# Kernel optimization log

Hardware: AMD Instinct MI355X
Metric: run time of the kernel (lower is better)

The kernel has to match this reference:

```python
import jax, jax.numpy as jnp
import numpy as np

B, D, H, W, K = 32, 256, 32, 32, 2048
BETA = 0.25
JSD_TS = 1.0


def setup_inputs() -> dict:
    key = jax.random.key(0)
    k1, k2 = jax.random.split(key)
    z = jax.random.normal(k1, (B, D, H, W), dtype=jnp.float32)
    # nn.Embedding(K, D) with uniform(-1/K, 1/K) init
    codebook = jax.random.uniform(k2, (K, D), minval=-1.0 / K, maxval=1.0 / K, dtype=jnp.float32)
    return {"z": z, "codebook": codebook, "i": 0, "it": 0}


def _vq_forward(z, codebook):
    b, d, h, w = z.shape
    # (b, d, h, w) -> (b*h*w, d)
    z_flat = jnp.transpose(z, (0, 2, 3, 1)).reshape(-1, d)
    # squared euclidean distances via sum-of-squares + matmul: (n, K)
    dist = (jnp.sum(z_flat * z_flat, axis=1, keepdims=True)
            + jnp.sum(codebook * codebook, axis=1)
            - 2.0 * (z_flat @ codebook.T))
    min_idx = jnp.argmin(dist, axis=1)                      # (n,)
    distance_prob = jax.nn.softmax(-dist / JSD_TS, axis=1)  # (n, K)
    z_q = codebook[min_idx]                                 # embedding gather (n, d)
    # VQ losses (normalize == 'none' so z_norm == z_flat)
    codebook_loss = jnp.mean((z_q - jax.lax.stop_gradient(z_flat)) ** 2)
    commitment_loss = jnp.mean((z_flat - jax.lax.stop_gradient(z_q)) ** 2)
    q_loss = codebook_loss + BETA * commitment_loss
    # straight-through estimator
    z_q = z_flat + jax.lax.stop_gradient(z_q - z_flat)
    z_q = jnp.transpose(z_q.reshape(b, h, w, d), (0, 3, 1, 2))
    return z_q, q_loss, distance_prob


def reference(z, codebook, i, it):
    # i, it are unused loop counters in the original forward (eval path)
    return _vq_forward(z, codebook)
```

## Files before the change

### kernel.cpp

```cpp
#include <hip/hip_runtime.h>
#include <stdint.h>

#define K_CODES 2048
#define DIM 256
#define NROWS 32768
#define ROWS_PER_BLOCK 16
#define THREADS 512
#define HW_STRIDE 1024
#define QLOSS_OFFSET 8388608
#define PROB_OFFSET 8388609ULL
#define ZB_PITCH 264
#define NBLOCKS (NROWS / ROWS_PER_BLOCK)
#define CPX (NBLOCKS / 8)

typedef short v8s __attribute__((ext_vector_type(8)));
typedef float v4f __attribute__((ext_vector_type(4)));
typedef __fp16 v2h __attribute__((ext_vector_type(2)));

__device__ __forceinline__ ushort f2bf(float x) {
    uint32_t u = __float_as_uint(x);
    return (ushort)((u + 0x7FFFu + ((u >> 16) & 1u)) >> 16);
}

__global__ void prep_kernel(const float* __restrict__ cb, ushort* __restrict__ cbb,
                            float* __restrict__ cnorm, float* __restrict__ qloss) {
    const int code = blockIdx.x;
    const int lane = threadIdx.x;
    float4 v = ((const float4*)(cb + code * DIM))[lane];
    ushort4 o;
    o.x = f2bf(v.x); o.y = f2bf(v.y); o.z = f2bf(v.z); o.w = f2bf(v.w);
    ((ushort4*)(cbb + code * DIM))[lane] = o;
    float ss = v.x * v.x + v.y * v.y + v.z * v.z + v.w * v.w;
    #pragma unroll
    for (int m = 32; m >= 1; m >>= 1) ss += __shfl_xor(ss, m, 64);
    if (lane == 0) cnorm[code] = ss;
    if (code == 0 && lane == 0) *qloss = 0.f;
}

__launch_bounds__(THREADS, 4)
__global__ void vq_kernel(const float* __restrict__ z, const float* __restrict__ cb,
                          const ushort* __restrict__ cbb, const float* __restrict__ cnorm,
                          float* __restrict__ out) {
    __shared__ float zf[DIM * 16];
    __shared__ ushort zb[ROWS_PER_BLOCK * ZB_PITCH];
    __shared__ float red_sum[8][16];
    __shared__ float red_val[8][16];
    __shared__ int   red_code[8][16];
    __shared__ float row_sum[16];
    __shared__ int   row_idx[16];
    __shared__ float lred[8];

    const int t = threadIdx.x;
    const int bid = ((int)blockIdx.x & 7) * CPX + ((int)blockIdx.x >> 3);
    const int n0 = bid * ROWS_PER_BLOCK;
    const int bb = n0 >> 10;
    const int hw = n0 & 1023;
    const float* zbase = z + (size_t)bb * (DIM * HW_STRIDE) + hw;

    #pragma unroll
    for (int j = 0; j < 2; ++j) {
        int i4 = t + j * THREADS;
        int d = i4 >> 2, m0 = (i4 & 3) << 2;
        float4 v = *(const float4*)(zbase + (size_t)d * HW_STRIDE + m0);
        *(float4*)&zf[d * 16 + m0] = v;
    }
    __syncthreads();
    #pragma unroll
    for (int j = 0; j < 4; ++j) {
        int i2 = t + j * THREADS;
        int m = i2 & 15, kp = i2 >> 4;
        float a0 = zf[(2 * kp) * 16 + m];
        float a1 = zf[(2 * kp + 1) * 16 + m];
        uint32_t pk = (uint32_t)f2bf(a0) | ((uint32_t)f2bf(a1) << 16);
        *(uint32_t*)&zb[m * ZB_PITCH + 2 * kp] = pk;
    }
    __syncthreads();

    const int wave = t >> 6, lane = t & 63;
    const int q = lane >> 4, lm = lane & 15;
    const int c0 = wave * 256;

    v8s afrag[8];
    const ushort* arow = &zb[lm * ZB_PITCH + q * 8];
    #pragma unroll
    for (int ks = 0; ks < 8; ++ks) afrag[ks] = *(const v8s*)(arow + ks * 32);

    float cnr[16];
    #pragma unroll
    for (int ct = 0; ct < 16; ++ct) cnr[ct] = cnorm[c0 + ct * 16 + lm];

    const ushort* bptr = cbb + (size_t)(c0 + lm) * DIM + q * 8;
    v8s bb0[8];
    #pragma unroll
    for (int ks = 0; ks < 8; ++ks) bb0[ks] = *(const v8s*)(bptr + ks * 32);

    v2h ep[32];
    float sume[4] = {0.f, 0.f, 0.f, 0.f};
    float bval[4] = {-1e30f, -1e30f, -1e30f, -1e30f};
    int   bcode[4] = {0, 0, 0, 0};
    #pragma unroll
    for (int ct = 0; ct < 16; ++ct) {
        v8s bb1[8];
        if (ct < 15) {
            const ushort* np = bptr + (size_t)(ct + 1) * (16 * DIM);
            #pragma unroll
            for (int ks = 0; ks < 8; ++ks) bb1[ks] = *(const v8s*)(np + ks * 32);
        }
        v4f a = {0.f, 0.f, 0.f, 0.f};
        #pragma unroll
        for (int ks = 0; ks < 8; ++ks)
            a = __builtin_amdgcn_mfma_f32_16x16x32_bf16(afrag[ks], bb0[ks], a, 0, 0, 0);
        const float cn = cnr[ct];
        const int code = c0 + ct * 16 + lm;
        #pragma unroll
        for (int r = 0; r < 4; ++r) {
            float l = 2.f * a[r] - cn;
            float ev = __expf(l);
            sume[r] += ev;
            if (l > bval[r]) { bval[r] = l; bcode[r] = code; }
            a[r] = ev;
        }
        ep[2 * ct]     = __builtin_amdgcn_cvt_pkrtz(a[0], a[1]);
        ep[2 * ct + 1] = __builtin_amdgcn_cvt_pkrtz(a[2], a[3]);
        #pragma unroll
        for (int ks = 0; ks < 8; ++ks) bb0[ks] = bb1[ks];
    }
    #pragma unroll
    for (int m = 1; m <= 8; m <<= 1) {
        #pragma unroll
        for (int r = 0; r < 4; ++r) {
            sume[r] += __shfl_xor(sume[r], m, 64);
            float v2 = __shfl_xor(bval[r], m, 64);
            int   c2 = __shfl_xor(bcode[r], m, 64);
            if (v2 > bval[r] || (v2 == bval[r] && c2 < bcode[r])) { bval[r] = v2; bcode[r] = c2; }
        }
    }
    if (lm == 0) {
        #pragma unroll
        for (int r = 0; r < 4; ++r) {
            red_sum[wave][q * 4 + r]  = sume[r];
            red_val[wave][q * 4 + r]  = bval[r];
            red_code[wave][q * 4 + r] = bcode[r];
        }
    }
    __syncthreads();
    if (t < 16) {
        float s = 0.f, bv = -1e30f;
        int bc = 0;
        #pragma unroll
        for (int w = 0; w < 8; ++w) {
            s += red_sum[w][t];
            float v = red_val[w][t];
            int   c = red_code[w][t];
            if (v > bv || (v == bv && c < bc)) { bv = v; bc = c; }
        }
        row_sum[t] = s;
        row_idx[t] = bc;
    }
    __syncthreads();

    float rinv[4];
    #pragma unroll
    for (int r = 0; r < 4; ++r) rinv[r] = 1.f / row_sum[q * 4 + r];
    float* prob = out + PROB_OFFSET;
    #pragma unroll
    for (int ct = 0; ct < 16; ++ct) {
        int col = c0 + ct * 16 + lm;
        float e0 = (float)ep[2 * ct][0];
        float e1 = (float)ep[2 * ct][1];
        float e2 = (float)ep[2 * ct + 1][0];
        float e3 = (float)ep[2 * ct + 1][1];
        size_t base = (size_t)(n0 + q * 4) * K_CODES + col;
        __builtin_nontemporal_store(e0 * rinv[0], prob + base);
        __builtin_nontemporal_store(e1 * rinv[1], prob + base + K_CODES);
        __builtin_nontemporal_store(e2 * rinv[2], prob + base + 2 * K_CODES);
        __builtin_nontemporal_store(e3 * rinv[3], prob + base + 3 * K_CODES);
    }

    float lacc = 0.f;
    #pragma unroll
    for (int j = 0; j < 2; ++j) {
        int i4 = t + j * THREADS;
        int d = i4 >> 2, m0 = (i4 & 3) << 2;
        float ov[4];
        #pragma unroll
        for (int i = 0; i < 4; ++i) {
            int m = m0 + i;
            float cv = cb[row_idx[m] * DIM + d];
            float zv = zf[d * 16 + m];
            float df = zv - cv;
            lacc += df * df;
            ov[i] = cv;
        }
        v4f o4 = {ov[0], ov[1], ov[2], ov[3]};
        __builtin_nontemporal_store(
            o4, (v4f*)(out + (size_t)bb * (DIM * HW_STRIDE) + hw + (size_t)d * HW_STRIDE + m0));
    }
    #pragma unroll
    for (int m = 32; m >= 1; m >>= 1) lacc += __shfl_xor(lacc, m, 64);
    if (lane == 0) lred[wave] = lacc;
    __syncthreads();
    if (t == 0) {
        float s = 0.f;
        #pragma unroll
        for (int w = 0; w < 8; ++w) s += lred[w];
        atomicAdd(out + QLOSS_OFFSET, s * (1.25f / 8388608.f));
    }
}

extern "C" void kernel_launch(void* const* d_in, const int* in_sizes, int n_in,
                              void* d_out, int out_size, void* d_ws, size_t ws_size,
                              hipStream_t stream) {
    const float* z  = (const float*)d_in[0];
    const float* cb = (const float*)d_in[1];
    float* out = (float*)d_out;
    ushort* cbb  = (ushort*)d_ws;
    float*  cnm  = (float*)((char*)d_ws + (size_t)K_CODES * DIM * sizeof(ushort));
    prep_kernel<<<K_CODES, 64, 0, stream>>>(cb, cbb, cnm, out + QLOSS_OFFSET);
    vq_kernel<<<NBLOCKS, THREADS, 0, stream>>>(z, cb, cbb, cnm, out);
}
```

Measured before the change: 643.6 us.

## Stage softmax exponentials in LDS for coalesced full-row probability stores

```diff
diff --git a/kernel.cpp b/kernel.cpp
--- a/kernel.cpp
+++ b/kernel.cpp
@@ -10,12 +10,13 @@
 #define QLOSS_OFFSET 8388608
 #define PROB_OFFSET 8388609ULL
 #define ZB_PITCH 264
+#define EP_PITCH 2052
 #define NBLOCKS (NROWS / ROWS_PER_BLOCK)
 #define CPX (NBLOCKS / 8)
 
 typedef short v8s __attribute__((ext_vector_type(8)));
 typedef float v4f __attribute__((ext_vector_type(4)));
-typedef __fp16 v2h __attribute__((ext_vector_type(2)));
+typedef __fp16 v4h __attribute__((ext_vector_type(4)));
 
 __device__ __forceinline__ ushort f2bf(float x) {
     uint32_t u = __float_as_uint(x);
@@ -41,7 +42,7 @@
 __global__ void vq_kernel(const float* __restrict__ z, const float* __restrict__ cb,
                           const ushort* __restrict__ cbb, const float* __restrict__ cnorm,
                           float* __restrict__ out) {
-    __shared__ float zf[DIM * 16];
+    __shared__ __align__(16) ushort eplds[ROWS_PER_BLOCK * EP_PITCH];
     __shared__ ushort zb[ROWS_PER_BLOCK * ZB_PITCH];
     __shared__ float red_sum[8][16];
     __shared__ float red_val[8][16];
@@ -57,11 +58,16 @@
     const int hw = n0 & 1023;
     const float* zbase = z + (size_t)bb * (DIM * HW_STRIDE) + hw;
 
+    float* zf = (float*)eplds;
+
+    float zrf[8];
     #pragma unroll
     for (int j = 0; j < 2; ++j) {
         int i4 = t + j * THREADS;
         int d = i4 >> 2, m0 = (i4 & 3) << 2;
         float4 v = *(const float4*)(zbase + (size_t)d * HW_STRIDE + m0);
+        zrf[4 * j + 0] = v.x; zrf[4 * j + 1] = v.y;
+        zrf[4 * j + 2] = v.z; zrf[4 * j + 3] = v.w;
         *(float4*)&zf[d * 16 + m0] = v;
     }
     __syncthreads();
@@ -85,43 +91,40 @@
     #pragma unroll
     for (int ks = 0; ks < 8; ++ks) afrag[ks] = *(const v8s*)(arow + ks * 32);
 
-    float cnr[16];
-    #pragma unroll
-    for (int ct = 0; ct < 16; ++ct) cnr[ct] = cnorm[c0 + ct * 16 + lm];
-
     const ushort* bptr = cbb + (size_t)(c0 + lm) * DIM + q * 8;
     v8s bb0[8];
     #pragma unroll
     for (int ks = 0; ks < 8; ++ks) bb0[ks] = *(const v8s*)(bptr + ks * 32);
-
-    v2h ep[32];
+    float cn0 = cnorm[c0 + lm];
+
+    __fp16* epf = (__fp16*)eplds;
     float sume[4] = {0.f, 0.f, 0.f, 0.f};
     float bval[4] = {-1e30f, -1e30f, -1e30f, -1e30f};
     int   bcode[4] = {0, 0, 0, 0};
     #pragma unroll
     for (int ct = 0; ct < 16; ++ct) {
         v8s bb1[8];
+        float cn1;
         if (ct < 15) {
             const ushort* np = bptr + (size_t)(ct + 1) * (16 * DIM);
             #pragma unroll
             for (int ks = 0; ks < 8; ++ks) bb1[ks] = *(const v8s*)(np + ks * 32);
+            cn1 = cnorm[c0 + (ct + 1) * 16 + lm];
         }
         v4f a = {0.f, 0.f, 0.f, 0.f};
         #pragma unroll
         for (int ks = 0; ks < 8; ++ks)
             a = __builtin_amdgcn_mfma_f32_16x16x32_bf16(afrag[ks], bb0[ks], a, 0, 0, 0);
-        const float cn = cnr[ct];
         const int code = c0 + ct * 16 + lm;
         #pragma unroll
         for (int r = 0; r < 4; ++r) {
-            float l = 2.f * a[r] - cn;
+            float l = 2.f * a[r] - cn0;
             float ev = __expf(l);
             sume[r] += ev;
             if (l > bval[r]) { bval[r] = l; bcode[r] = code; }
-            a[r] = ev;
-        }
-        ep[2 * ct]     = __builtin_amdgcn_cvt_pkrtz(a[0], a[1]);
-        ep[2 * ct + 1] = __builtin_amdgcn_cvt_pkrtz(a[2], a[3]);
+            epf[(q * 4 + r) * EP_PITCH + code] = (__fp16)ev;
+        }
+        cn0 = cn1;
         #pragma unroll
         for (int ks = 0; ks < 8; ++ks) bb0[ks] = bb1[ks];
     }
@@ -159,22 +162,22 @@
     }
     __syncthreads();
 
-    float rinv[4];
-    #pragma unroll
-    for (int r = 0; r < 4; ++r) rinv[r] = 1.f / row_sum[q * 4 + r];
+    float cv[8];
+    #pragma unroll
+    for (int j = 0; j < 2; ++j) {
+        int i4 = t + j * THREADS;
+        int d = i4 >> 2, m0 = (i4 & 3) << 2;
+        #pragma unroll
+        for (int i = 0; i < 4; ++i) cv[4 * j + i] = cb[row_idx[m0 + i] * DIM + d];
+    }
+
     float* prob = out + PROB_OFFSET;
     #pragma unroll
-    for (int ct = 0; ct < 16; ++ct) {
-        int col = c0 + ct * 16 + lm;
-        float e0 = (float)ep[2 * ct][0];
-        float e1 = (float)ep[2 * ct][1];
-        float e2 = (float)ep[2 * ct + 1][0];
-        float e3 = (float)ep[2 * ct + 1][1];
-        size_t base = (size_t)(n0 + q * 4) * K_CODES + col;
-        __builtin_nontemporal_store(e0 * rinv[0], prob + base);
-        __builtin_nontemporal_store(e1 * rinv[1], prob + base + K_CODES);
-        __builtin_nontemporal_store(e2 * rinv[2], prob + base + 2 * K_CODES);
-        __builtin_nontemporal_store(e3 * rinv[3], prob + base + 3 * K_CODES);
+    for (int rr = 0; rr < ROWS_PER_BLOCK; ++rr) {
+        float rs = 1.f / row_sum[rr];
+        v4h e = *(const v4h*)&epf[rr * EP_PITCH + t * 4];
+        v4f o = { e[0] * rs, e[1] * rs, e[2] * rs, e[3] * rs };
+        *(v4f*)(prob + (size_t)(n0 + rr) * K_CODES + t * 4) = o;
     }
 
     float lacc = 0.f;
@@ -185,16 +188,13 @@
         float ov[4];
         #pragma unroll
         for (int i = 0; i < 4; ++i) {
-            int m = m0 + i;
-            float cv = cb[row_idx[m] * DIM + d];
-            float zv = zf[d * 16 + m];
-            float df = zv - cv;
+            float cvv = cv[4 * j + i];
+            float df = zrf[4 * j + i] - cvv;
             lacc += df * df;
-            ov[i] = cv;
+            ov[i] = cvv;
         }
         v4f o4 = {ov[0], ov[1], ov[2], ov[3]};
-        __builtin_nontemporal_store(
-            o4, (v4f*)(out + (size_t)bb * (DIM * HW_STRIDE) + hw + (size_t)d * HW_STRIDE + m0));
+        *(v4f*)(out + (size_t)bb * (DIM * HW_STRIDE) + hw + (size_t)d * HW_STRIDE + m0) = o4;
     }
     #pragma unroll
     for (int m = 32; m >= 1; m >>= 1) lacc += __shfl_xor(lacc, m, 64);
```

After: 571.9 us. -11.1%, faster.
